# Kernel optimization log

Hardware: AMD Instinct MI355X
Metric: run time of the kernel (lower is better)

The kernel has to match this reference:

```python
import jax, jax.numpy as jnp
import numpy as np

T, D, E, K = 16384, 2048, 128, 8

def setup_inputs() -> dict:
    key = jax.random.key(0)
    k1, k2 = jax.random.split(key)
    hidden_states = jax.random.normal(k1, (T, D), dtype=jnp.float32)
    weight = jax.random.normal(k2, (E, D), dtype=jnp.float32) * 0.02
    return {"hidden_states": hidden_states, "weight": weight}

def reference(hidden_states, weight):
    # (T, D) @ (D, E) -> (T, E) router logits
    x = hidden_states.reshape(-1, weight.shape[1])
    logits = jnp.einsum('td,ed->te', x, weight)
    # softmax in float32 over experts
    router_logits = jax.nn.softmax(logits.astype(jnp.float32), axis=-1)
    # top-k selection + renormalization so selected weights sum to 1
    router_weights, router_indices = jax.lax.top_k(router_logits, K)
    router_weights = router_weights / jnp.sum(router_weights, axis=-1, keepdims=True)
    return (router_logits, router_weights, router_indices)
```

## Files before the change

kernel.cpp:

```cpp
#include <hip/hip_runtime.h>
#include <math.h>


constexpr int T = 16384;
constexpr int D = 2048;
constexpr int E = 128;
constexpr int K = 8;

constexpr int BM  = 32;
constexpr int NS  = 5;
constexpr int NP  = D / 64;

typedef int i32x4  __attribute__((ext_vector_type(4)));
typedef int i32x16 __attribute__((ext_vector_type(16)));

__device__ __forceinline__ void slice5(float x, float c, float ic, int out[NS]) {
    float r = x;
#pragma unroll
    for (int s = 0; s < NS; ++s) {
        float q = rintf(r * c);
        out[s] = (int)q;
        r = fmaf(q, -ic, r);
        c *= 128.f;
        ic *= (1.f / 128.f);
    }
}

__global__ __launch_bounds__(256)
void w_slice(const float* __restrict__ W, signed char* __restrict__ Ws)
{
    const int e  = blockIdx.x >> 1;
    const int k0 = ((blockIdx.x & 1) << 10) | (threadIdx.x << 2);
    float4 v = *(const float4*)(W + (size_t)e * D + k0);
    int b0[NS], b1[NS], b2[NS], b3[NS];
    slice5(v.x, 512.f, 1.f / 512.f, b0);
    slice5(v.y, 512.f, 1.f / 512.f, b1);
    slice5(v.z, 512.f, 1.f / 512.f, b2);
    slice5(v.w, 512.f, 1.f / 512.f, b3);
#pragma unroll
    for (int s = 0; s < NS; ++s) {
        unsigned pk = (unsigned)(b0[s] & 255)        | ((unsigned)(b1[s] & 255) << 8) |
                      ((unsigned)(b2[s] & 255) << 16) | ((unsigned)(b3[s] & 255) << 24);
        *(int*)(Ws + (size_t)s * E * D + (size_t)e * D + k0) = (int)pk;
    }
}

__global__ __launch_bounds__(256, 2)
void router_fused(const float* __restrict__ X,
                  const signed char* __restrict__ Ws,
                  float* __restrict__ out)
{
    __shared__ __align__(16) signed char As[2][2][NS][2][BM][16];
    __shared__ double Ld[BM][E];

    const int tid = threadIdx.x;
    const long t0 = (long)blockIdx.x * BM;

    const int ar = tid >> 3;
    const int ac = (tid & 7) << 2;
    const float* Xp = X + (t0 + ar) * (long)D + ac;

    const int l  = tid & 63;
    const int wv = tid >> 6;
    const int mr = l & 31;
    const int mh = l >> 5;

    const size_t wbase = (size_t)(wv * 32 + mr) * D + (size_t)mh * 16;
    const i32x4* wp0 = (const i32x4*)(Ws + 0UL * E * D + wbase);
    const i32x4* wp1 = (const i32x4*)(Ws + 1UL * E * D + wbase);
    const i32x4* wp2 = (const i32x4*)(Ws + 2UL * E * D + wbase);
    const i32x4* wp3 = (const i32x4*)(Ws + 3UL * E * D + wbase);
    const i32x4* wp4 = (const i32x4*)(Ws + 4UL * E * D + wbase);

    i32x16 acc0 = {}, acc1 = {}, acc2 = {}, acc3 = {}, acc4 = {};

    auto stageChunk = [&](const float4& v, int buf, int chn) {
        int bx0[NS], bx1[NS], bx2[NS], bx3[NS];
        slice5(v.x, 16.f, 1.f / 16.f, bx0);
        slice5(v.y, 16.f, 1.f / 16.f, bx1);
        slice5(v.z, 16.f, 1.f / 16.f, bx2);
        slice5(v.w, 16.f, 1.f / 16.f, bx3);
        char* dst = (char*)&As[buf][chn][0][ac >> 4][ar][ac & 15];
#pragma unroll
        for (int s = 0; s < NS; ++s) {
            unsigned pk = (unsigned)(bx0[s] & 255)        | ((unsigned)(bx1[s] & 255) << 8) |
                          ((unsigned)(bx2[s] & 255) << 16) | ((unsigned)(bx3[s] & 255) << 24);
            *(int*)(dst + s * 1024) = (int)pk;
        }
    };

    auto mstep = [&](int buf, int chn,
                     const i32x4& b0, const i32x4& b1, const i32x4& b2,
                     const i32x4& b3, const i32x4& b4) {
        i32x4 a0 = *(const i32x4*)&As[buf][chn][0][mh][mr][0];
        i32x4 a1 = *(const i32x4*)&As[buf][chn][1][mh][mr][0];
        i32x4 a2 = *(const i32x4*)&As[buf][chn][2][mh][mr][0];
        i32x4 a3 = *(const i32x4*)&As[buf][chn][3][mh][mr][0];
        i32x4 a4 = *(const i32x4*)&As[buf][chn][4][mh][mr][0];
        acc0 = __builtin_amdgcn_mfma_i32_32x32x32_i8(a0, b0, acc0, 0, 0, 0);
        acc1 = __builtin_amdgcn_mfma_i32_32x32x32_i8(a0, b1, acc1, 0, 0, 0);
        acc1 = __builtin_amdgcn_mfma_i32_32x32x32_i8(a1, b0, acc1, 0, 0, 0);
        acc2 = __builtin_amdgcn_mfma_i32_32x32x32_i8(a0, b2, acc2, 0, 0, 0);
        acc2 = __builtin_amdgcn_mfma_i32_32x32x32_i8(a1, b1, acc2, 0, 0, 0);
        acc2 = __builtin_amdgcn_mfma_i32_32x32x32_i8(a2, b0, acc2, 0, 0, 0);
        acc3 = __builtin_amdgcn_mfma_i32_32x32x32_i8(a0, b3, acc3, 0, 0, 0);
        acc3 = __builtin_amdgcn_mfma_i32_32x32x32_i8(a1, b2, acc3, 0, 0, 0);
        acc3 = __builtin_amdgcn_mfma_i32_32x32x32_i8(a2, b1, acc3, 0, 0, 0);
        acc3 = __builtin_amdgcn_mfma_i32_32x32x32_i8(a3, b0, acc3, 0, 0, 0);
        acc4 = __builtin_amdgcn_mfma_i32_32x32x32_i8(a0, b4, acc4, 0, 0, 0);
        acc4 = __builtin_amdgcn_mfma_i32_32x32x32_i8(a1, b3, acc4, 0, 0, 0);
        acc4 = __builtin_amdgcn_mfma_i32_32x32x32_i8(a2, b2, acc4, 0, 0, 0);
        acc4 = __builtin_amdgcn_mfma_i32_32x32x32_i8(a3, b1, acc4, 0, 0, 0);
        acc4 = __builtin_amdgcn_mfma_i32_32x32x32_i8(a4, b0, acc4, 0, 0, 0);
    };

    float4 xs0 = *(const float4*)(Xp);
    float4 xs1 = *(const float4*)(Xp + 32);
    stageChunk(xs0, 0, 0);
    stageChunk(xs1, 0, 1);
    xs0 = *(const float4*)(Xp + 64);
    xs1 = *(const float4*)(Xp + 96);
    __syncthreads();

    for (int p = 0; p < NP; ++p) {
        const int cur = p & 1;

        i32x4 b0 = wp0[4 * p],     b1 = wp1[4 * p],     b2 = wp2[4 * p],
              b3 = wp3[4 * p],     b4 = wp4[4 * p];
        i32x4 c0 = wp0[4 * p + 2], c1 = wp1[4 * p + 2], c2 = wp2[4 * p + 2],
              c3 = wp3[4 * p + 2], c4 = wp4[4 * p + 2];

        if (p < NP - 1) {
            stageChunk(xs0, cur ^ 1, 0);
            stageChunk(xs1, cur ^ 1, 1);
        }
        if (p < NP - 2) {
            xs0 = *(const float4*)(Xp + (2 * p + 4) * 32);
            xs1 = *(const float4*)(Xp + (2 * p + 5) * 32);
        }

        mstep(cur, 0, b0, b1, b2, b3, b4);
        mstep(cur, 1, c0, c1, c2, c3, c4);

        __syncthreads();
    }

#pragma unroll
    for (int r = 0; r < 16; ++r) {
        const int row = (r & 3) + 8 * (r >> 2) + 4 * mh;
        const double lg = (double)acc0[r] * 0x1p-13
                        + (double)acc1[r] * 0x1p-20
                        + (double)acc2[r] * 0x1p-27
                        + (double)acc3[r] * 0x1p-34
                        + (double)acc4[r] * 0x1p-41;
        Ld[row][wv * 32 + mr] = lg;
    }
    __syncthreads();

    float* outL  = out;
    float* outWt = out + (long)T * E;
    float* outId = outWt + (long)T * K;
    const int tx = tid & 15;

    for (int rep = 0; rep < 2; ++rep) {
        const int tt = (tid >> 4) + rep * 16;
        const long t = t0 + tt;

        double acc[8];
#pragma unroll
        for (int j = 0; j < 8; ++j) acc[j] = Ld[tt][(tx << 3) + j];

        double m = acc[0];
#pragma unroll
        for (int j = 1; j < 8; ++j) m = fmax(m, acc[j]);
#pragma unroll
        for (int mask = 1; mask <= 8; mask <<= 1)
            m = fmax(m, __shfl_xor(m, mask, 64));

        float e[8]; float s = 0.f;
#pragma unroll
        for (int j = 0; j < 8; ++j) { e[j] = __expf((float)(acc[j] - m)); s += e[j]; }
#pragma unroll
        for (int mask = 1; mask <= 8; mask <<= 1)
            s += __shfl_xor(s, mask, 64);
        const float inv = 1.f / s;

        float4 st0 = {e[0] * inv, e[1] * inv, e[2] * inv, e[3] * inv};
        float4 st1 = {e[4] * inv, e[5] * inv, e[6] * inv, e[7] * inv};
        *(float4*)&outL[t * E + (tx << 3)]     = st0;
        *(float4*)&outL[t * E + (tx << 3) + 4] = st1;

        double v[8];
#pragma unroll
        for (int j = 0; j < 8; ++j) v[j] = acc[j];

        float pk[K]; int ik[K]; float tsum = 0.f;
#pragma unroll
        for (int r = 0; r < K; ++r) {
            double bv = -1.0e300; int bi = 0x7fffffff;
#pragma unroll
            for (int j = 0; j < 8; ++j) {
                const int idx = (tx << 3) + j;
                const bool better = (v[j] > bv) || (v[j] == bv && idx < bi);
                bv = better ? v[j] : bv;
                bi = better ? idx : bi;
            }
#pragma unroll
            for (int mask = 1; mask <= 8; mask <<= 1) {
                const double ov = __shfl_xor(bv, mask, 64);
                const int    oi = __shfl_xor(bi, mask, 64);
                const bool better = (ov > bv) || (ov == bv && oi < bi);
                bv = better ? ov : bv;
                bi = better ? oi : bi;
            }
            const float pw = __expf((float)(bv - m)) * inv;
            pk[r] = pw; ik[r] = bi; tsum += pw;
            const bool own  = ((bi >> 3) == tx);
            const int  slot = bi & 7;
#pragma unroll
            for (int j = 0; j < 8; ++j)
                v[j] = (own && j == slot) ? -1.0e300 : v[j];
        }

        if (tx == 0) {
            const float rinv = 1.f / tsum;
#pragma unroll
            for (int r = 0; r < K; ++r) {
                outWt[t * K + r] = pk[r] * rinv;
                outId[t * K + r] = (float)ik[r];
            }
        }
    }
}

extern "C" void kernel_launch(void* const* d_in, const int* in_sizes, int n_in,
                              void* d_out, int out_size, void* d_ws, size_t ws_size,
                              hipStream_t stream)
{
    const float* X = (const float*)d_in[0];
    const float* W = (const float*)d_in[1];
    float* out = (float*)d_out;
    signed char* Ws = (signed char*)d_ws;

    w_slice<<<dim3(E * 2), dim3(256), 0, stream>>>(W, Ws);
    router_fused<<<dim3(T / BM), dim3(256), 0, stream>>>(X, Ws, out);
}
```

Measured before the change: 277.2 us.

## Switch to 16x16x64 int8 MFMA with 512-thread blocks and perm packing

Replaces the 32x32x32 int8 MFMA tiling with 16x16x64 MFMA tiles and splits the 128 experts across 8 waves of 16 experts each, so each block now runs 512 threads. The shared-memory A layout is changed to match, each thread stages one float4 per 64-wide K step instead of two, and byte packing now uses v_perm instead of shift/or chains. The epilogue gives each thread one token instead of two. The aim is more waves in flight and finer-grained MFMA scheduling, in exchange for more register and LDS pressure per CU and more synchronisation across a larger block.

```diff
diff --git a/kernel.cpp b/kernel.cpp
--- a/kernel.cpp
+++ b/kernel.cpp
@@ -7,12 +7,13 @@
 constexpr int E = 128;
 constexpr int K = 8;
 
-constexpr int BM  = 32;
-constexpr int NS  = 5;
-constexpr int NP  = D / 64;
-
-typedef int i32x4  __attribute__((ext_vector_type(4)));
-typedef int i32x16 __attribute__((ext_vector_type(16)));
+constexpr int BM = 32;
+constexpr int NS = 5;
+constexpr int NB = D / 64;
+
+typedef int i32x4 __attribute__((ext_vector_type(4)));
+
+#define MFI8(A, B, C) C = __builtin_amdgcn_mfma_i32_16x16x64_i8(A, B, C, 0, 0, 0)
 
 __device__ __forceinline__ void slice5(float x, float c, float ic, int out[NS]) {
     float r = x;
@@ -39,121 +40,106 @@
     slice5(v.w, 512.f, 1.f / 512.f, b3);
 #pragma unroll
     for (int s = 0; s < NS; ++s) {
-        unsigned pk = (unsigned)(b0[s] & 255)        | ((unsigned)(b1[s] & 255) << 8) |
-                      ((unsigned)(b2[s] & 255) << 16) | ((unsigned)(b3[s] & 255) << 24);
+        unsigned lo = __builtin_amdgcn_perm((unsigned)b1[s], (unsigned)b0[s], 0x00000400u);
+        unsigned hi = __builtin_amdgcn_perm((unsigned)b3[s], (unsigned)b2[s], 0x00000400u);
+        unsigned pk = __builtin_amdgcn_perm(hi, lo, 0x05040100u);
         *(int*)(Ws + (size_t)s * E * D + (size_t)e * D + k0) = (int)pk;
     }
 }
 
-__global__ __launch_bounds__(256, 2)
+__global__ __launch_bounds__(512, 4)
 void router_fused(const float* __restrict__ X,
                   const signed char* __restrict__ Ws,
                   float* __restrict__ out)
 {
-    __shared__ __align__(16) signed char As[2][2][NS][2][BM][16];
+    __shared__ __align__(16) signed char As[2][NS][2][4][16][16];
     __shared__ double Ld[BM][E];
 
     const int tid = threadIdx.x;
     const long t0 = (long)blockIdx.x * BM;
 
-    const int ar = tid >> 3;
-    const int ac = (tid & 7) << 2;
+    const int ar = tid >> 4;
+    const int ac = (tid & 15) << 2;
     const float* Xp = X + (t0 + ar) * (long)D + ac;
 
     const int l  = tid & 63;
     const int wv = tid >> 6;
-    const int mr = l & 31;
-    const int mh = l >> 5;
-
-    const size_t wbase = (size_t)(wv * 32 + mr) * D + (size_t)mh * 16;
-    const i32x4* wp0 = (const i32x4*)(Ws + 0UL * E * D + wbase);
-    const i32x4* wp1 = (const i32x4*)(Ws + 1UL * E * D + wbase);
-    const i32x4* wp2 = (const i32x4*)(Ws + 2UL * E * D + wbase);
-    const i32x4* wp3 = (const i32x4*)(Ws + 3UL * E * D + wbase);
-    const i32x4* wp4 = (const i32x4*)(Ws + 4UL * E * D + wbase);
-
-    i32x16 acc0 = {}, acc1 = {}, acc2 = {}, acc3 = {}, acc4 = {};
-
-    auto stageChunk = [&](const float4& v, int buf, int chn) {
-        int bx0[NS], bx1[NS], bx2[NS], bx3[NS];
-        slice5(v.x, 16.f, 1.f / 16.f, bx0);
-        slice5(v.y, 16.f, 1.f / 16.f, bx1);
-        slice5(v.z, 16.f, 1.f / 16.f, bx2);
-        slice5(v.w, 16.f, 1.f / 16.f, bx3);
-        char* dst = (char*)&As[buf][chn][0][ac >> 4][ar][ac & 15];
+    const int er = l & 15;
+    const int kg = l >> 4;
+
+    const signed char* Wp = Ws + (size_t)(wv * 16 + er) * D + (size_t)kg * 16;
+
+    i32x4 p00 = {}, p01 = {}, p02 = {}, p03 = {}, p04 = {};
+    i32x4 p10 = {}, p11 = {}, p12 = {}, p13 = {}, p14 = {};
+
+    auto stage = [&](const float4& v, int buf) {
+        int q0[NS], q1[NS], q2[NS], q3[NS];
+        slice5(v.x, 16.f, 1.f / 16.f, q0);
+        slice5(v.y, 16.f, 1.f / 16.f, q1);
+        slice5(v.z, 16.f, 1.f / 16.f, q2);
+        slice5(v.w, 16.f, 1.f / 16.f, q3);
+        int* dst = (int*)&As[buf][0][ar >> 4][ac >> 4][ar & 15][ac & 15];
 #pragma unroll
         for (int s = 0; s < NS; ++s) {
-            unsigned pk = (unsigned)(bx0[s] & 255)        | ((unsigned)(bx1[s] & 255) << 8) |
-                          ((unsigned)(bx2[s] & 255) << 16) | ((unsigned)(bx3[s] & 255) << 24);
-            *(int*)(dst + s * 1024) = (int)pk;
+            unsigned lo = __builtin_amdgcn_perm((unsigned)q1[s], (unsigned)q0[s], 0x00000400u);
+            unsigned hi = __builtin_amdgcn_perm((unsigned)q3[s], (unsigned)q2[s], 0x00000400u);
+            unsigned pk = __builtin_amdgcn_perm(hi, lo, 0x05040100u);
+            dst[s * 512] = (int)pk;
         }
     };
 
-    auto mstep = [&](int buf, int chn,
-                     const i32x4& b0, const i32x4& b1, const i32x4& b2,
-                     const i32x4& b3, const i32x4& b4) {
-        i32x4 a0 = *(const i32x4*)&As[buf][chn][0][mh][mr][0];
-        i32x4 a1 = *(const i32x4*)&As[buf][chn][1][mh][mr][0];
-        i32x4 a2 = *(const i32x4*)&As[buf][chn][2][mh][mr][0];
-        i32x4 a3 = *(const i32x4*)&As[buf][chn][3][mh][mr][0];
-        i32x4 a4 = *(const i32x4*)&As[buf][chn][4][mh][mr][0];
-        acc0 = __builtin_amdgcn_mfma_i32_32x32x32_i8(a0, b0, acc0, 0, 0, 0);
-        acc1 = __builtin_amdgcn_mfma_i32_32x32x32_i8(a0, b1, acc1, 0, 0, 0);
-        acc1 = __builtin_amdgcn_mfma_i32_32x32x32_i8(a1, b0, acc1, 0, 0, 0);
-        acc2 = __builtin_amdgcn_mfma_i32_32x32x32_i8(a0, b2, acc2, 0, 0, 0);
-        acc2 = __builtin_amdgcn_mfma_i32_32x32x32_i8(a1, b1, acc2, 0, 0, 0);
-        acc2 = __builtin_amdgcn_mfma_i32_32x32x32_i8(a2, b0, acc2, 0, 0, 0);
-        acc3 = __builtin_amdgcn_mfma_i32_32x32x32_i8(a0, b3, acc3, 0, 0, 0);
-        acc3 = __builtin_amdgcn_mfma_i32_32x32x32_i8(a1, b2, acc3, 0, 0, 0);
-        acc3 = __builtin_amdgcn_mfma_i32_32x32x32_i8(a2, b1, acc3, 0, 0, 0);
-        acc3 = __builtin_amdgcn_mfma_i32_32x32x32_i8(a3, b0, acc3, 0, 0, 0);
-        acc4 = __builtin_amdgcn_mfma_i32_32x32x32_i8(a0, b4, acc4, 0, 0, 0);
-        acc4 = __builtin_amdgcn_mfma_i32_32x32x32_i8(a1, b3, acc4, 0, 0, 0);
-        acc4 = __builtin_amdgcn_mfma_i32_32x32x32_i8(a2, b2, acc4, 0, 0, 0);
-        acc4 = __builtin_amdgcn_mfma_i32_32x32x32_i8(a3, b1, acc4, 0, 0, 0);
-        acc4 = __builtin_amdgcn_mfma_i32_32x32x32_i8(a4, b0, acc4, 0, 0, 0);
+    auto tileStep = [&](int buf, int tl,
+                        const i32x4& b0, const i32x4& b1, const i32x4& b2,
+                        const i32x4& b3, const i32x4& b4,
+                        i32x4& d0, i32x4& d1, i32x4& d2, i32x4& d3, i32x4& d4) {
+        const signed char* ap = &As[buf][0][tl][0][0][0] + l * 16;
+        i32x4 a0 = *(const i32x4*)(ap);
+        i32x4 a1 = *(const i32x4*)(ap + 2048);
+        i32x4 a2 = *(const i32x4*)(ap + 4096);
+        i32x4 a3 = *(const i32x4*)(ap + 6144);
+        i32x4 a4 = *(const i32x4*)(ap + 8192);
+        MFI8(a0, b0, d0);
+        MFI8(a0, b1, d1); MFI8(a1, b0, d1);
+        MFI8(a0, b2, d2); MFI8(a1, b1, d2); MFI8(a2, b0, d2);
+        MFI8(a0, b3, d3); MFI8(a1, b2, d3); MFI8(a2, b1, d3); MFI8(a3, b0, d3);
+        MFI8(a0, b4, d4); MFI8(a1, b3, d4); MFI8(a2, b2, d4); MFI8(a3, b1, d4);
+        MFI8(a4, b0, d4);
     };
 
-    float4 xs0 = *(const float4*)(Xp);
-    float4 xs1 = *(const float4*)(Xp + 32);
-    stageChunk(xs0, 0, 0);
-    stageChunk(xs1, 0, 1);
-    xs0 = *(const float4*)(Xp + 64);
-    xs1 = *(const float4*)(Xp + 96);
+    float4 xv = *(const float4*)(Xp);
+    stage(xv, 0);
+    xv = *(const float4*)(Xp + 64);
     __syncthreads();
 
-    for (int p = 0; p < NP; ++p) {
+    for (int p = 0; p < NB; ++p) {
         const int cur = p & 1;
-
-        i32x4 b0 = wp0[4 * p],     b1 = wp1[4 * p],     b2 = wp2[4 * p],
-              b3 = wp3[4 * p],     b4 = wp4[4 * p];
-        i32x4 c0 = wp0[4 * p + 2], c1 = wp1[4 * p + 2], c2 = wp2[4 * p + 2],
-              c3 = wp3[4 * p + 2], c4 = wp4[4 * p + 2];
-
-        if (p < NP - 1) {
-            stageChunk(xs0, cur ^ 1, 0);
-            stageChunk(xs1, cur ^ 1, 1);
-        }
-        if (p < NP - 2) {
-            xs0 = *(const float4*)(Xp + (2 * p + 4) * 32);
-            xs1 = *(const float4*)(Xp + (2 * p + 5) * 32);
-        }
-
-        mstep(cur, 0, b0, b1, b2, b3, b4);
-        mstep(cur, 1, c0, c1, c2, c3, c4);
+        const long kb = (long)p * 64;
+
+        i32x4 b0 = *(const i32x4*)(Wp + 0UL * E * D + kb);
+        i32x4 b1 = *(const i32x4*)(Wp + 1UL * E * D + kb);
+        i32x4 b2 = *(const i32x4*)(Wp + 2UL * E * D + kb);
+        i32x4 b3 = *(const i32x4*)(Wp + 3UL * E * D + kb);
+        i32x4 b4 = *(const i32x4*)(Wp + 4UL * E * D + kb);
+
+        if (p < NB - 1) stage(xv, cur ^ 1);
+        if (p < NB - 2) xv = *(const float4*)(Xp + (p + 2) * 64);
+
+        tileStep(cur, 0, b0, b1, b2, b3, b4, p00, p01, p02, p03, p04);
+        tileStep(cur, 1, b0, b1, b2, b3, b4, p10, p11, p12, p13, p14);
 
         __syncthreads();
     }
 
 #pragma unroll
-    for (int r = 0; r < 16; ++r) {
-        const int row = (r & 3) + 8 * (r >> 2) + 4 * mh;
-        const double lg = (double)acc0[r] * 0x1p-13
-                        + (double)acc1[r] * 0x1p-20
-                        + (double)acc2[r] * 0x1p-27
-                        + (double)acc3[r] * 0x1p-34
-                        + (double)acc4[r] * 0x1p-41;
-        Ld[row][wv * 32 + mr] = lg;
+    for (int r = 0; r < 4; ++r) {
+        const int row0 = kg * 4 + r;
+        const int col  = wv * 16 + er;
+        Ld[row0][col]      = (double)p00[r] * 0x1p-13 + (double)p01[r] * 0x1p-20
+                           + (double)p02[r] * 0x1p-27 + (double)p03[r] * 0x1p-34
+                           + (double)p04[r] * 0x1p-41;
+        Ld[row0 + 16][col] = (double)p10[r] * 0x1p-13 + (double)p11[r] * 0x1p-20
+                           + (double)p12[r] * 0x1p-27 + (double)p13[r] * 0x1p-34
+                           + (double)p14[r] * 0x1p-41;
     }
     __syncthreads();
 
@@ -161,74 +147,71 @@
     float* outWt = out + (long)T * E;
     float* outId = outWt + (long)T * K;
     const int tx = tid & 15;
-
-    for (int rep = 0; rep < 2; ++rep) {
-        const int tt = (tid >> 4) + rep * 16;
-        const long t = t0 + tt;
-
-        double acc[8];
-#pragma unroll
-        for (int j = 0; j < 8; ++j) acc[j] = Ld[tt][(tx << 3) + j];
-
-        double m = acc[0];
-#pragma unroll
-        for (int j = 1; j < 8; ++j) m = fmax(m, acc[j]);
-#pragma unroll
-        for (int mask = 1; mask <= 8; mask <<= 1)
-            m = fmax(m, __shfl_xor(m, mask, 64));
-
-        float e[8]; float s = 0.f;
-#pragma unroll
-        for (int j = 0; j < 8; ++j) { e[j] = __expf((float)(acc[j] - m)); s += e[j]; }
-#pragma unroll
-        for (int mask = 1; mask <= 8; mask <<= 1)
-            s += __shfl_xor(s, mask, 64);
-        const float inv = 1.f / s;
-
-        float4 st0 = {e[0] * inv, e[1] * inv, e[2] * inv, e[3] * inv};
-        float4 st1 = {e[4] * inv, e[5] * inv, e[6] * inv, e[7] * inv};
-        *(float4*)&outL[t * E + (tx << 3)]     = st0;
-        *(float4*)&outL[t * E + (tx << 3) + 4] = st1;
-
-        double v[8];
-#pragma unroll
-        for (int j = 0; j < 8; ++j) v[j] = acc[j];
-
-        float pk[K]; int ik[K]; float tsum = 0.f;
+    const int tt = tid >> 4;
+    const long t = t0 + tt;
+
+    double acc[8];
+#pragma unroll
+    for (int j = 0; j < 8; ++j) acc[j] = Ld[tt][(tx << 3) + j];
+
+    double m = acc[0];
+#pragma unroll
+    for (int j = 1; j < 8; ++j) m = fmax(m, acc[j]);
+#pragma unroll
+    for (int mask = 1; mask <= 8; mask <<= 1)
+        m = fmax(m, __shfl_xor(m, mask, 64));
+
+    float e[8]; float s = 0.f;
+#pragma unroll
+    for (int j = 0; j < 8; ++j) { e[j] = __expf((float)(acc[j] - m)); s += e[j]; }
+#pragma unroll
+    for (int mask = 1; mask <= 8; mask <<= 1)
+        s += __shfl_xor(s, mask, 64);
+    const float inv = 1.f / s;
+
+    float4 st0 = {e[0] * inv, e[1] * inv, e[2] * inv, e[3] * inv};
+    float4 st1 = {e[4] * inv, e[5] * inv, e[6] * inv, e[7] * inv};
+    *(float4*)&outL[t * E + (tx << 3)]     = st0;
+    *(float4*)&outL[t * E + (tx << 3) + 4] = st1;
+
+    double v[8];
+#pragma unroll
+    for (int j = 0; j < 8; ++j) v[j] = acc[j];
+
+    float pk[K]; int ik[K]; float tsum = 0.f;
+#pragma unroll
+    for (int r = 0; r < K; ++r) {
+        double bv = -1.0e300; int bi = 0x7fffffff;
+#pragma unroll
+        for (int j = 0; j < 8; ++j) {
+            const int idx = (tx << 3) + j;
+            const bool better = (v[j] > bv) || (v[j] == bv && idx < bi);
+            bv = better ? v[j] : bv;
+            bi = better ? idx : bi;
+        }
+#pragma unroll
+        for (int mask = 1; mask <= 8; mask <<= 1) {
+            const double ov = __shfl_xor(bv, mask, 64);
+            const int    oi = __shfl_xor(bi, mask, 64);
+            const bool better = (ov > bv) || (ov == bv && oi < bi);
+            bv = better ? ov : bv;
+            bi = better ? oi : bi;
+        }
+        const float pw = __expf((float)(bv - m)) * inv;
+        pk[r] = pw; ik[r] = bi; tsum += pw;
+        const bool own  = ((bi >> 3) == tx);
+        const int  slot = bi & 7;
+#pragma unroll
+        for (int j = 0; j < 8; ++j)
+            v[j] = (own && j == slot) ? -1.0e300 : v[j];
+    }
+
+    if (tx == 0) {
+        const float rinv = 1.f / tsum;
 #pragma unroll
         for (int r = 0; r < K; ++r) {
-            double bv = -1.0e300; int bi = 0x7fffffff;
-#pragma unroll
-            for (int j = 0; j < 8; ++j) {
-                const int idx = (tx << 3) + j;
-                const bool better = (v[j] > bv) || (v[j] == bv && idx < bi);
-                bv = better ? v[j] : bv;
-                bi = better ? idx : bi;
-            }
-#pragma unroll
-            for (int mask = 1; mask <= 8; mask <<= 1) {
-                const double ov = __shfl_xor(bv, mask, 64);
-                const int    oi = __shfl_xor(bi, mask, 64);
-                const bool better = (ov > bv) || (ov == bv && oi < bi);
-                bv = better ? ov : bv;
-                bi = better ? oi : bi;
-            }
-            const float pw = __expf((float)(bv - m)) * inv;
-            pk[r] = pw; ik[r] = bi; tsum += pw;
-            const bool own  = ((bi >> 3) == tx);
-            const int  slot = bi & 7;
-#pragma unroll
-            for (int j = 0; j < 8; ++j)
-                v[j] = (own && j == slot) ? -1.0e300 : v[j];
-        }
-
-        if (tx == 0) {
-            const float rinv = 1.f / tsum;
-#pragma unroll
-            for (int r = 0; r < K; ++r) {
-                outWt[t * K + r] = pk[r] * rinv;
-                outId[t * K + r] = (float)ik[r];
-            }
+            outWt[t * K + r] = pk[r] * rinv;
+            outId[t * K + r] = (float)ik[r];
         }
     }
 }
@@ -243,5 +226,5 @@
     signed char* Ws = (signed char*)d_ws;
 
     w_slice<<<dim3(E * 2), dim3(256), 0, stream>>>(W, Ws);
-    router_fused<<<dim3(T / BM), dim3(256), 0, stream>>>(X, Ws, out);
-}
+    router_fused<<<dim3(T / BM), dim3(512), 0, stream>>>(X, Ws, out);
+}
```

New measurement: 266.8 us. -3.8%, faster.
